# Kernel optimization log

Measured on AMD Instinct MI355X. Metric: run time of the kernel, lower is better.

Reference implementation:

```python
import jax, jax.numpy as jnp
import numpy as np
from jax import lax

B, L, D_MODEL = 4, 1024, 512
D_STATE, D_CONV, D_INNER = 16, 4, 2 * D_MODEL


def setup_inputs() -> dict:
    key = jax.random.key(0)
    ks = jax.random.split(key, 8)
    s = 0.02
    x = jax.random.normal(ks[0], (B, L, D_MODEL), dtype=jnp.float32)
    W_in = jax.random.normal(ks[1], (D_MODEL, 2 * D_INNER), dtype=jnp.float32) * s
    conv_w = jax.random.normal(ks[2], (D_INNER, 1, D_CONV), dtype=jnp.float32) * s  # OIH, depthwise
    conv_b = jnp.zeros((D_INNER,), jnp.float32)
    W_x = jax.random.normal(ks[3], (D_INNER, 2 * D_STATE), dtype=jnp.float32) * s
    W_dt = jax.random.normal(ks[4], (D_INNER, D_INNER), dtype=jnp.float32) * s
    b_dt = jnp.zeros((D_INNER,), jnp.float32)
    # A_log = -logspace(log10(0.001), log10(1.0), d_state); used directly as A in the scan
    A_log = -jnp.logspace(np.log10(1e-3), 0.0, D_STATE, dtype=jnp.float32)
    D_skip = jnp.ones((D_INNER,), jnp.float32) * 0.1
    W_out = jax.random.normal(ks[5], (D_INNER, D_MODEL), dtype=jnp.float32) * s
    gamma = jnp.ones((D_MODEL,), jnp.float32)
    beta = jnp.zeros((D_MODEL,), jnp.float32)
    return dict(x=x, W_in=W_in, conv_w=conv_w, conv_b=conv_b, W_x=W_x, W_dt=W_dt,
                b_dt=b_dt, A_log=A_log, D_skip=D_skip, W_out=W_out, gamma=gamma, beta=beta)


def _mamba_forward(x, W_in, conv_w, conv_b, W_x, W_dt, b_dt, A_log, D_skip, W_out, gamma, beta):
    x = jnp.clip(x, -10.0, 10.0)
    x_and_res = x @ W_in                                  # [B, L, 2*d_inner]
    xp, res = jnp.split(x_and_res, 2, axis=-1)
    # Depthwise causal conv1d: torch pads d_conv-1 both sides then slices [:L] -> left-pad only.
    xt = jnp.transpose(xp, (0, 2, 1))                     # [B, d_inner, L]
    xc = lax.conv_general_dilated(xt, conv_w, window_strides=(1,),
                                  padding=[(D_CONV - 1, 0)],
                                  dimension_numbers=('NCH', 'OIH', 'NCH'),
                                  feature_group_count=D_INNER)
    xc = xc + conv_b[None, :, None]
    xc = jax.nn.silu(jnp.transpose(xc, (0, 2, 1)))        # [B, L, d_inner]
    ssm = xc @ W_x                                        # [B, L, 2*d_state]
    Bm, Cm = jnp.split(ssm, 2, axis=-1)                   # each [B, L, d_state]
    delta = xc @ W_dt + b_dt                              # [B, L, d_inner] (no softplus in source)

    # Selective scan over time (sequential recurrence)
    def step(h, inp):
        u_t, d_t, B_t, C_t = inp                          # [B,I], [B,I], [B,S], [B,S]
        dA = jnp.exp(jnp.clip(d_t[:, :, None] * A_log, -5.0, 5.0))   # [B, I, S]
        h = dA * h + (d_t[:, :, None] * B_t[:, None, :]) * u_t[:, :, None]
        y = jnp.einsum('bis,bs->bi', h, C_t)
        return h, y

    tm = lambda a: jnp.swapaxes(a, 0, 1)                  # time-major
    h0 = jnp.zeros((x.shape[0], D_INNER, D_STATE), xc.dtype)
    _, ys = lax.scan(step, h0, (tm(xc), tm(delta), tm(Bm), tm(Cm)))
    y = jnp.swapaxes(ys, 0, 1) + xc * D_skip              # D skip connection

    y = y * jax.nn.silu(res)                              # gating
    out = y @ W_out
    r = out + x                                           # residual
    mu = jnp.mean(r, axis=-1, keepdims=True)
    var = jnp.var(r, axis=-1, keepdims=True)
    return gamma * (r - mu) / jnp.sqrt(var + 1e-5) + beta


def reference(x, W_in, conv_w, conv_b, W_x, W_dt, b_dt, A_log, D_skip, W_out, gamma, beta):
    return _mamba_forward(x, W_in, conv_w, conv_b, W_x, W_dt, b_dt, A_log, D_skip, W_out, gamma, beta)
```

## Files before the change

### kernel.cpp

```cpp
#include <hip/hip_runtime.h>
#include <hip/hip_bf16.h>

typedef __hip_bfloat16 bf16;
typedef unsigned short ushort_t;
typedef unsigned int uint_t;
typedef __attribute__((ext_vector_type(8))) __bf16 bf16x8;
typedef __attribute__((ext_vector_type(8))) ushort_t u16x8;
typedef __attribute__((ext_vector_type(4))) float f32x4;

#define BB 4
#define LL 1024
#define DM 512
#define DS 16
#define DI 1024
#define ROWS 4096
#define NC 64
#define CT 16
#define NDTX 1152

__device__ __forceinline__ float b2f(bf16 v) { return __bfloat162float(v); }

__device__ __forceinline__ float load_flag(const void* src, int i, int isbf)
{
    return isbf ? b2f(((const bf16*)src)[i]) : ((const float*)src)[i];
}

__device__ __forceinline__ ushort_t f2b_bits(float v)
{
    bf16 t = __float2bfloat16(v);
    return *(ushort_t*)&t;
}

__device__ __forceinline__ float bits2f(ushort_t u)
{
    uint_t w = ((uint_t)u) << 16;
    return __uint_as_float(w);
}

__device__ __forceinline__ int detect_local(const ushort_t* wdt)
{
    __shared__ int bad;
    if (threadIdx.x == 0) bad = 0;
    __syncthreads();
    ushort_t u = wdt[threadIdx.x & 255];
    if (((u >> 7) & 0xFF) >= 127) atomicAdd(&bad, 1);
    __syncthreads();
    return (bad <= 8) ? 1 : 0;
}

__global__ __launch_bounds__(256)
void prep_all(const void* x, const void* Win, const void* Wdt, const void* Wx,
              const void* Wout, const void* cw, const void* cb, const void* Alog,
              const void* Dsk, const void* gam, const void* bet, const void* bdt,
              bf16* __restrict__ xbf, bf16* __restrict__ WtIn,
              bf16* __restrict__ WtDtx, bf16* __restrict__ WtOut,
              float* __restrict__ ccw, float* __restrict__ ccb,
              float* __restrict__ cAlg, float* __restrict__ cDsk,
              float* __restrict__ cgam, float* __restrict__ cbet,
              float* __restrict__ bdtx)
{
    const int isbf = detect_local((const ushort_t*)Wdt);
    int blk = blockIdx.x;

    if (blk < 2048) {
        int idx = blk * 256 + threadIdx.x;
        float v[4];
        if (isbf) {
            uint2 raw = ((const uint2*)x)[idx];
            v[0] = __uint_as_float(raw.x << 16);
            v[1] = __uint_as_float(raw.x & 0xFFFF0000u);
            v[2] = __uint_as_float(raw.y << 16);
            v[3] = __uint_as_float(raw.y & 0xFFFF0000u);
        } else {
            float4 raw = ((const float4*)x)[idx];
            v[0] = raw.x; v[1] = raw.y; v[2] = raw.z; v[3] = raw.w;
        }
        uint_t b0, b1;
        b0 = f2b_bits(fminf(fmaxf(v[0], -10.f), 10.f))
           | ((uint_t)f2b_bits(fminf(fmaxf(v[1], -10.f), 10.f)) << 16);
        b1 = f2b_bits(fminf(fmaxf(v[2], -10.f), 10.f))
           | ((uint_t)f2b_bits(fminf(fmaxf(v[3], -10.f), 10.f)) << 16);
        uint2 ow; ow.x = b0; ow.y = b1;
        ((uint2*)xbf)[idx] = ow;
    } else if (blk < 4640) {
        int tb = blk - 2048;
        const void* src; bf16* dst; int K, Nsrc, tpr;
        if (tb < 1024)      { src = Win;  dst = WtIn;               K = 512;  Nsrc = 2048; tpr = 64; }
        else if (tb < 2048) { tb -= 1024; src = Wdt;  dst = WtDtx;  K = 1024; Nsrc = 1024; tpr = 32; }
        else if (tb < 2080) { tb -= 2048; src = Wx;   dst = WtDtx + 1024 * 1024; K = 1024; Nsrc = 32; tpr = 1; }
        else                { tb -= 2080; src = Wout; dst = WtOut;  K = 1024; Nsrc = 512;  tpr = 16; }
        int k0 = (tb / tpr) * 32, n0 = (tb % tpr) * 32;

        __shared__ float tile[32][33];
        int tx = threadIdx.x & 31, ty = threadIdx.x >> 5;
        #pragma unroll
        for (int j = 0; j < 4; ++j)
            tile[ty + 8 * j][tx] = load_flag(src, (k0 + ty + 8 * j) * Nsrc + n0 + tx, isbf);
        __syncthreads();
        #pragma unroll
        for (int j = 0; j < 4; ++j)
            dst[(size_t)(n0 + ty + 8 * j) * K + k0 + tx] = __float2bfloat16(tile[tx][ty + 8 * j]);
    } else {
        int i = (blk - 4640) * 256 + threadIdx.x;
        if (i < 4096)        ccw[i] = load_flag(cw, i, isbf);
        else if (i < 5120)   ccb[i - 4096] = load_flag(cb, i - 4096, isbf);
        else if (i < 5136)   cAlg[i - 5120] = load_flag(Alog, i - 5120, isbf);
        else if (i < 6160)   cDsk[i - 5136] = load_flag(Dsk, i - 5136, isbf);
        else if (i < 6672)   cgam[i - 6160] = load_flag(gam, i - 6160, isbf);
        else if (i < 7184)   cbet[i - 6672] = load_flag(bet, i - 6672, isbf);
        else if (i < 8336) {
            int j = i - 7184;
            bdtx[j] = (j < DI) ? load_flag(bdt, j, isbf) : 0.f;
        } else if (i < 106640) {
            (WtDtx + 1056 * 1024)[i - 8336] = __float2bfloat16(0.f);
        }
    }
}

__device__ __forceinline__ void gload16(const bf16* g, ushort_t* l)
{
    __builtin_amdgcn_global_load_lds(
        (const __attribute__((address_space(1))) void*)g,
        (__attribute__((address_space(3))) void*)l, 16, 0, 0);
}

template <int TM, int TN, bool OBF>
__global__ __launch_bounds__(256)
void gemm_mfma(const bf16* __restrict__ A, const bf16* __restrict__ Bt,
               const float* __restrict__ bias, void* __restrict__ Cv,
               int M, int N, int K)
{
    constexpr int MI = TM / 32, NJ = TN / 32;
    constexpr int NQA = TM * 8 / 256;
    constexpr int NQB = TN * 8 / 256;
    __shared__ ushort_t As[TM * 64];
    __shared__ ushort_t Bs[TN * 64];

    const int tid = threadIdx.x;
    const int lane = tid & 63;
    const int w = tid >> 6;
    const int wr = w >> 1, wc = w & 1;
    const int m0 = blockIdx.y * TM;
    const int n0 = blockIdx.x * TN;

    const bf16* gA[NQA]; ushort_t* lA[NQA];
    #pragma unroll
    for (int q = 0; q < NQA; ++q) {
        int p = q * 256 + tid;
        int row = p >> 3, kc = ((p & 7) - row) & 7;
        gA[q] = A + (size_t)(m0 + row) * K + kc * 8;
        lA[q] = &As[(q * 256 + w * 64) * 8];
    }
    const bf16* gB[NQB]; ushort_t* lB[NQB];
    #pragma unroll
    for (int q = 0; q < NQB; ++q) {
        int p = q * 256 + tid;
        int row = p >> 3, kc = ((p & 7) - row) & 7;
        gB[q] = Bt + (size_t)(n0 + row) * K + kc * 8;
        lB[q] = &Bs[(q * 256 + w * 64) * 8];
    }

    f32x4 acc[MI][NJ];
    #pragma unroll
    for (int i = 0; i < MI; ++i)
        #pragma unroll
        for (int j = 0; j < NJ; ++j)
            acc[i][j] = (f32x4){0.f, 0.f, 0.f, 0.f};

    const int ko = lane >> 4;
    const int ml = lane & 15;

    for (int k0 = 0; k0 < K; k0 += 64) {
        #pragma unroll
        for (int q = 0; q < NQA; ++q) gload16(gA[q] + k0, lA[q]);
        #pragma unroll
        for (int q = 0; q < NQB; ++q) gload16(gB[q] + k0, lB[q]);
        __syncthreads();

        #pragma unroll
        for (int half = 0; half < 2; ++half) {
            bf16x8 af[MI], bfr[NJ];
            #pragma unroll
            for (int i = 0; i < MI; ++i) {
                int m = wr * (TM / 2) + i * 16 + ml;
                af[i] = *(const bf16x8*)&As[(m * 8 + ((half * 4 + ko + m) & 7)) * 8];
            }
            #pragma unroll
            for (int j = 0; j < NJ; ++j) {
                int n = wc * (TN / 2) + j * 16 + ml;
                bfr[j] = *(const bf16x8*)&Bs[(n * 8 + ((half * 4 + ko + n) & 7)) * 8];
            }
            #pragma unroll
            for (int i = 0; i < MI; ++i)
                #pragma unroll
                for (int j = 0; j < NJ; ++j)
                    acc[i][j] = __builtin_amdgcn_mfma_f32_16x16x32_bf16(
                        af[i], bfr[j], acc[i][j], 0, 0, 0);
        }
        __syncthreads();
    }

    const int rq = lane >> 4;
    #pragma unroll
    for (int j = 0; j < NJ; ++j) {
        int n = n0 + wc * (TN / 2) + j * 16 + ml;
        float bv = bias ? bias[n] : 0.f;
        #pragma unroll
        for (int i = 0; i < MI; ++i) {
            int mb = m0 + wr * (TM / 2) + i * 16 + rq * 4;
            #pragma unroll
            for (int r = 0; r < 4; ++r) {
                float v = acc[i][j][r] + bv;
                if (OBF) ((bf16*)Cv)[(size_t)(mb + r) * N + n] = __float2bfloat16(v);
                else     ((float*)Cv)[(size_t)(mb + r) * N + n] = v;
            }
        }
    }
}

__global__ __launch_bounds__(256)
void conv_silu(const bf16* __restrict__ xrb, const float* __restrict__ cw,
               const float* __restrict__ cb, bf16* __restrict__ xcb)
{
    int idx = blockIdx.x * 256 + threadIdx.x;
    int i = (idx & 127) * 8;
    int row = idx >> 7;
    int t = row & (LL - 1);

    const u16x8 zv = {0, 0, 0, 0, 0, 0, 0, 0};
    const ushort_t* base = (const ushort_t*)(xrb) + (size_t)row * 2048 + i;
    u16x8 r3 = *(const u16x8*)base;
    u16x8 r2 = (t >= 1) ? *(const u16x8*)(base - 2048) : zv;
    u16x8 r1 = (t >= 2) ? *(const u16x8*)(base - 4096) : zv;
    u16x8 r0 = (t >= 3) ? *(const u16x8*)(base - 6144) : zv;

    u16x8 out;
    #pragma unroll
    for (int k = 0; k < 8; ++k) {
        float4 w = ((const float4*)cw)[i + k];
        float acc = cb[i + k];
        acc = fmaf(bits2f(r0[k]), w.x, acc);
        acc = fmaf(bits2f(r1[k]), w.y, acc);
        acc = fmaf(bits2f(r2[k]), w.z, acc);
        acc = fmaf(bits2f(r3[k]), w.w, acc);
        out[k] = f2b_bits(acc / (1.f + __expf(-acc)));
    }
    *(u16x8*)((ushort_t*)xcb + (size_t)row * DI + i) = out;
}

__global__ __launch_bounds__(1024)
void scan_fused(const bf16* __restrict__ xcb, const bf16* __restrict__ dlx,
                const bf16* __restrict__ xrb, const float* __restrict__ A_log,
                const float* __restrict__ Dskip, bf16* __restrict__ ybf)
{
    __shared__ uint_t lsum[DS * NC * 16];

    const int tid = threadIdx.x;
    const int b = blockIdx.x >> 6;
    const int ch0 = (blockIdx.x & 63) << 4;
    const int chl = tid & 15;
    const int c = tid >> 4;
    const int i = ch0 + chl;

    float a[DS];
    #pragma unroll
    for (int s = 0; s < DS; ++s) a[s] = A_log[s];

    const int row0 = b * LL + c * CT;
    float h[DS] = {};
    float p[DS];
    #pragma unroll
    for (int s = 0; s < DS; ++s) p[s] = 1.f;

    for (int t = 0; t < CT; ++t) {
        const size_t row = row0 + t;
        float d = bits2f(((const ushort_t*)dlx)[row * NDTX + i]);
        float u = bits2f(((const ushort_t*)xcb)[row * DI + i]);
        float du = d * u;
        const u16x8* sp = (const u16x8*)(dlx + row * NDTX + 1024);
        u16x8 B0 = sp[0], B1 = sp[1];
        #pragma unroll
        for (int s = 0; s < DS; ++s) {
            float e = fminf(fmaxf(d * a[s], -5.f), 5.f);
            float dA = __expf(e);
            float Bv = bits2f(s < 8 ? B0[s] : B1[s - 8]);
            h[s] = fmaf(dA, h[s], du * Bv);
            p[s] *= dA;
        }
    }
    #pragma unroll
    for (int s = 0; s < DS; ++s)
        lsum[s * 1024 + tid] = (uint_t)f2b_bits(p[s]) | ((uint_t)f2b_bits(h[s]) << 16);
    __syncthreads();

    if (tid < 256) {
        int cl = tid & 15, s = tid >> 4;
        float hh = 0.f;
        for (int cc = 0; cc < NC; ++cc) {
            int off = s * 1024 + cc * 16 + cl;
            uint_t wrd = lsum[off];
            float pp = bits2f((ushort_t)(wrd & 0xFFFF));
            float qq = bits2f((ushort_t)(wrd >> 16));
            lsum[off] = (uint_t)f2b_bits(hh);
            hh = fmaf(pp, hh, qq);
        }
    }
    __syncthreads();

    #pragma unroll
    for (int s = 0; s < DS; ++s) h[s] = bits2f((ushort_t)lsum[s * 1024 + tid]);

    const float dsk = Dskip[i];
    for (int t = 0; t < CT; ++t) {
        const size_t row = row0 + t;
        float d = bits2f(((const ushort_t*)dlx)[row * NDTX + i]);
        float u = bits2f(((const ushort_t*)xcb)[row * DI + i]);
        float du = d * u;
        const u16x8* sp = (const u16x8*)(dlx + row * NDTX + 1024);
        u16x8 B0 = sp[0], B1 = sp[1], C0 = sp[2], C1 = sp[3];
        float y = 0.f;
        #pragma unroll
        for (int s = 0; s < DS; ++s) {
            float e = fminf(fmaxf(d * a[s], -5.f), 5.f);
            float dA = __expf(e);
            float Bv = bits2f(s < 8 ? B0[s] : B1[s - 8]);
            float Cv = bits2f(s < 8 ? C0[s] : C1[s - 8]);
            h[s] = fmaf(dA, h[s], du * Bv);
            y = fmaf(h[s], Cv, y);
        }
        float res = bits2f(((const ushort_t*)xrb)[row * 2048 + DI + i]);
        float g = res / (1.f + __expf(-res));
        ybf[row * DI + i] = __float2bfloat16((y + u * dsk) * g);
    }
}

__global__ __launch_bounds__(256)
void ln_kernel(const float* __restrict__ outp, const void* __restrict__ xsrc,
               const void* __restrict__ wdt_probe,
               const float* __restrict__ gamma, const float* __restrict__ beta,
               void* __restrict__ out)
{
    const int isbf = detect_local((const ushort_t*)wdt_probe);
    const int row = blockIdx.x;
    const int tid = threadIdx.x;

    float r[2];
    float sum = 0.f, ss = 0.f;
    #pragma unroll
    for (int q = 0; q < 2; ++q) {
        int j = tid + q * 256;
        float xv = load_flag(xsrc, row * DM + j, isbf);
        xv = fminf(fmaxf(xv, -10.f), 10.f);
        float v = outp[(size_t)row * DM + j] + xv;
        r[q] = v;
        sum += v;
        ss = fmaf(v, v, ss);
    }
    #pragma unroll
    for (int off = 32; off >= 1; off >>= 1) {
        sum += __shfl_down(sum, off);
        ss  += __shfl_down(ss, off);
    }
    __shared__ float s1[4], s2[4];
    __shared__ float stats[2];
    int wid = tid >> 6, lane = tid & 63;
    if (lane == 0) { s1[wid] = sum; s2[wid] = ss; }
    __syncthreads();
    if (tid == 0) {
        float S = s1[0] + s1[1] + s1[2] + s1[3];
        float Qq = s2[0] + s2[1] + s2[2] + s2[3];
        float mean = S / DM;
        float var = Qq / DM - mean * mean;
        stats[0] = mean;
        stats[1] = rsqrtf(var + 1e-5f);
    }
    __syncthreads();
    float mean = stats[0], rstd = stats[1];
    #pragma unroll
    for (int q = 0; q < 2; ++q) {
        int j = tid + q * 256;
        float v = (r[q] - mean) * rstd * gamma[j] + beta[j];
        size_t o = (size_t)row * DM + j;
        if (isbf) ((bf16*)out)[o] = __float2bfloat16(v);
        else      ((float*)out)[o] = v;
    }
}

extern "C" void kernel_launch(void* const* d_in, const int* in_sizes, int n_in,
                              void* d_out, int out_size, void* d_ws, size_t ws_size,
                              hipStream_t stream)
{
    float* W = (float*)d_ws;
    float* ccw  = W;
    float* ccb  = ccw  + 4096;
    float* cAlg = ccb  + 1024;
    float* cDsk = cAlg + 16;
    float* cgam = cDsk + 1024;
    float* cbet = cgam + 512;
    float* bdtx = cbet + 512;
    float* outp = bdtx + 1152;
    bf16*  xbf  = (bf16*)(outp + 2097152);
    bf16*  xrb  = xbf  + 2097152;
    bf16*  xcb  = xrb  + 8388608;
    bf16*  ybf  = xcb  + 4194304;
    bf16*  dlx  = ybf  + 4194304;
    bf16*  WtIn = dlx  + 4718592;
    bf16*  WtDtx= WtIn + 1048576;
    bf16*  WtOut= WtDtx+ 1179648;

    prep_all<<<5057, 256, 0, stream>>>(
        d_in[0], d_in[1], d_in[5], d_in[4], d_in[9], d_in[2], d_in[3],
        d_in[7], d_in[8], d_in[10], d_in[11], d_in[6],
        xbf, WtIn, WtDtx, WtOut, ccw, ccb, cAlg, cDsk, cgam, cbet, bdtx);

    gemm_mfma<64, 128, true><<<dim3(2048 / 128, ROWS / 64), 256, 0, stream>>>(
        xbf, WtIn, nullptr, xrb, ROWS, 2048, 512);

    conv_silu<<<ROWS * DI / 8 / 256, 256, 0, stream>>>(xrb, ccw, ccb, xcb);

    gemm_mfma<64, 128, true><<<dim3(NDTX / 128, ROWS / 64), 256, 0, stream>>>(
        xcb, WtDtx, bdtx, dlx, ROWS, NDTX, DI);

    scan_fused<<<256, 1024, 0, stream>>>(xcb, dlx, xrb, cAlg, cDsk, ybf);

    gemm_mfma<64, 64, false><<<dim3(DM / 64, ROWS / 64), 256, 0, stream>>>(
        ybf, WtOut, nullptr, outp, ROWS, DM, DI);

    ln_kernel<<<ROWS, 256, 0, stream>>>(outp, d_in[0], d_in[5], cgam, cbet, d_out);
}
```

Measured before the change: 218.0 us.

## Store intermediates channel-major so scan reads contiguous time vectors; split dt/ssm GEMMs

The in-projection and dt GEMMs now write transposed (channel-major) bf16 outputs. The conv kernel reads these along time, and it emits both channel-major and row-major copies through an LDS transpose. The dt projection and the B/C projection become separate GEMMs. The scan loads 16 timesteps of delta, u and the gate as vector loads instead of strided scalar reads. This trades coalesced row stores in the GEMM epilogue for 8-byte strided transposed stores, and adds an extra small GEMM launch and a duplicate xc buffer.

```diff
diff --git a/kernel.cpp b/kernel.cpp
--- a/kernel.cpp
+++ b/kernel.cpp
@@ -6,6 +6,7 @@
 typedef unsigned int uint_t;
 typedef __attribute__((ext_vector_type(8))) __bf16 bf16x8;
 typedef __attribute__((ext_vector_type(8))) ushort_t u16x8;
+typedef __attribute__((ext_vector_type(4))) ushort_t u16x4;
 typedef __attribute__((ext_vector_type(4))) float f32x4;
 
 #define BB 4
@@ -16,7 +17,6 @@
 #define ROWS 4096
 #define NC 64
 #define CT 16
-#define NDTX 1152
 
 __device__ __forceinline__ float b2f(bf16 v) { return __bfloat162float(v); }
 
@@ -51,13 +51,14 @@
 __global__ __launch_bounds__(256)
 void prep_all(const void* x, const void* Win, const void* Wdt, const void* Wx,
               const void* Wout, const void* cw, const void* cb, const void* Alog,
-              const void* Dsk, const void* gam, const void* bet, const void* bdt,
+              const void* Dsk, const void* gam, const void* bet, const void* bdtin,
               bf16* __restrict__ xbf, bf16* __restrict__ WtIn,
-              bf16* __restrict__ WtDtx, bf16* __restrict__ WtOut,
+              bf16* __restrict__ WtDt, bf16* __restrict__ WtSsm,
+              bf16* __restrict__ WtOut,
               float* __restrict__ ccw, float* __restrict__ ccb,
               float* __restrict__ cAlg, float* __restrict__ cDsk,
               float* __restrict__ cgam, float* __restrict__ cbet,
-              float* __restrict__ bdtx)
+              float* __restrict__ bdt)
 {
     const int isbf = detect_local((const ushort_t*)Wdt);
     int blk = blockIdx.x;
@@ -85,10 +86,10 @@
     } else if (blk < 4640) {
         int tb = blk - 2048;
         const void* src; bf16* dst; int K, Nsrc, tpr;
-        if (tb < 1024)      { src = Win;  dst = WtIn;               K = 512;  Nsrc = 2048; tpr = 64; }
-        else if (tb < 2048) { tb -= 1024; src = Wdt;  dst = WtDtx;  K = 1024; Nsrc = 1024; tpr = 32; }
-        else if (tb < 2080) { tb -= 2048; src = Wx;   dst = WtDtx + 1024 * 1024; K = 1024; Nsrc = 32; tpr = 1; }
-        else                { tb -= 2080; src = Wout; dst = WtOut;  K = 1024; Nsrc = 512;  tpr = 16; }
+        if (tb < 1024)      { src = Win;  dst = WtIn;  K = 512;  Nsrc = 2048; tpr = 64; }
+        else if (tb < 2048) { tb -= 1024; src = Wdt;  dst = WtDt;  K = 1024; Nsrc = 1024; tpr = 32; }
+        else if (tb < 2080) { tb -= 2048; src = Wx;   dst = WtSsm; K = 1024; Nsrc = 32;   tpr = 1; }
+        else                { tb -= 2080; src = Wout; dst = WtOut; K = 1024; Nsrc = 512;  tpr = 16; }
         int k0 = (tb / tpr) * 32, n0 = (tb % tpr) * 32;
 
         __shared__ float tile[32][33];
@@ -108,12 +109,8 @@
         else if (i < 6160)   cDsk[i - 5136] = load_flag(Dsk, i - 5136, isbf);
         else if (i < 6672)   cgam[i - 6160] = load_flag(gam, i - 6160, isbf);
         else if (i < 7184)   cbet[i - 6672] = load_flag(bet, i - 6672, isbf);
-        else if (i < 8336) {
-            int j = i - 7184;
-            bdtx[j] = (j < DI) ? load_flag(bdt, j, isbf) : 0.f;
-        } else if (i < 106640) {
-            (WtDtx + 1056 * 1024)[i - 8336] = __float2bfloat16(0.f);
-        }
+        else if (i < 8208)   bdt[i - 7184] = load_flag(bdtin, i - 7184, isbf);
+        else if (i < 40976)  (WtSsm + 32 * 1024)[i - 8208] = __float2bfloat16(0.f);
     }
 }
 
@@ -124,7 +121,7 @@
         (__attribute__((address_space(3))) void*)l, 16, 0, 0);
 }
 
-template <int TM, int TN, bool OBF>
+template <int TM, int TN, bool OBF, bool OT>
 __global__ __launch_bounds__(256)
 void gemm_mfma(const bf16* __restrict__ A, const bf16* __restrict__ Bt,
                const float* __restrict__ bias, void* __restrict__ Cv,
@@ -208,50 +205,81 @@
         #pragma unroll
         for (int i = 0; i < MI; ++i) {
             int mb = m0 + wr * (TM / 2) + i * 16 + rq * 4;
-            #pragma unroll
-            for (int r = 0; r < 4; ++r) {
-                float v = acc[i][j][r] + bv;
-                if (OBF) ((bf16*)Cv)[(size_t)(mb + r) * N + n] = __float2bfloat16(v);
-                else     ((float*)Cv)[(size_t)(mb + r) * N + n] = v;
+            if (OT) {
+                u16x4 pk;
+                #pragma unroll
+                for (int r = 0; r < 4; ++r)
+                    pk[r] = f2b_bits(acc[i][j][r] + bv);
+                *(u16x4*)((ushort_t*)Cv + (size_t)n * M + mb) = pk;
+            } else {
+                #pragma unroll
+                for (int r = 0; r < 4; ++r) {
+                    float v = acc[i][j][r] + bv;
+                    if (OBF) ((bf16*)Cv)[(size_t)(mb + r) * N + n] = __float2bfloat16(v);
+                    else     ((float*)Cv)[(size_t)(mb + r) * N + n] = v;
+                }
             }
         }
     }
 }
 
 __global__ __launch_bounds__(256)
-void conv_silu(const bf16* __restrict__ xrb, const float* __restrict__ cw,
-               const float* __restrict__ cb, bf16* __restrict__ xcb)
-{
-    int idx = blockIdx.x * 256 + threadIdx.x;
-    int i = (idx & 127) * 8;
-    int row = idx >> 7;
-    int t = row & (LL - 1);
-
-    const u16x8 zv = {0, 0, 0, 0, 0, 0, 0, 0};
-    const ushort_t* base = (const ushort_t*)(xrb) + (size_t)row * 2048 + i;
-    u16x8 r3 = *(const u16x8*)base;
-    u16x8 r2 = (t >= 1) ? *(const u16x8*)(base - 2048) : zv;
-    u16x8 r1 = (t >= 2) ? *(const u16x8*)(base - 4096) : zv;
-    u16x8 r0 = (t >= 3) ? *(const u16x8*)(base - 6144) : zv;
-
-    u16x8 out;
-    #pragma unroll
-    for (int k = 0; k < 8; ++k) {
-        float4 w = ((const float4*)cw)[i + k];
-        float acc = cb[i + k];
-        acc = fmaf(bits2f(r0[k]), w.x, acc);
-        acc = fmaf(bits2f(r1[k]), w.y, acc);
-        acc = fmaf(bits2f(r2[k]), w.z, acc);
-        acc = fmaf(bits2f(r3[k]), w.w, acc);
-        out[k] = f2b_bits(acc / (1.f + __expf(-acc)));
-    }
-    *(u16x8*)((ushort_t*)xcb + (size_t)row * DI + i) = out;
+void conv_silu(const bf16* __restrict__ xrbT, const float* __restrict__ cw,
+               const float* __restrict__ cb, bf16* __restrict__ xcT,
+               bf16* __restrict__ xc)
+{
+    __shared__ ushort_t tile[64 * 72];
+    const int blk = blockIdx.x;
+    const int ch0 = (blk & 15) * 64;
+    const int T0b = (blk >> 4) * 64;
+    const int lc = threadIdx.x >> 2, tg = threadIdx.x & 3;
+    const int i = ch0 + lc;
+    const int T0 = T0b + tg * 16;
+
+    const ushort_t* base = (const ushort_t*)xrbT + (size_t)i * ROWS + T0;
+    u16x8 m0 = *(const u16x8*)base;
+    u16x8 m1 = *(const u16x8*)(base + 8);
+    u16x8 pv = {0, 0, 0, 0, 0, 0, 0, 0};
+    if ((T0 & (LL - 1)) != 0) pv = *(const u16x8*)(base - 8);
+
+    float4 w = ((const float4*)cw)[i];
+    float bs = cb[i];
+    float xm3 = bits2f(pv[5]), xm2 = bits2f(pv[6]), xm1 = bits2f(pv[7]);
+    u16x8 o0, o1;
+    #pragma unroll
+    for (int tt = 0; tt < 16; ++tt) {
+        float x0 = bits2f(tt < 8 ? m0[tt] : m1[tt - 8]);
+        float acc = bs;
+        acc = fmaf(xm3, w.x, acc);
+        acc = fmaf(xm2, w.y, acc);
+        acc = fmaf(xm1, w.z, acc);
+        acc = fmaf(x0,  w.w, acc);
+        ushort_t ob = f2b_bits(acc / (1.f + __expf(-acc)));
+        if (tt < 8) o0[tt] = ob; else o1[tt - 8] = ob;
+        xm3 = xm2; xm2 = xm1; xm1 = x0;
+    }
+    ushort_t* dt = (ushort_t*)xcT + (size_t)i * ROWS + T0;
+    *(u16x8*)dt = o0;
+    *(u16x8*)(dt + 8) = o1;
+    *(u16x8*)&tile[lc * 72 + tg * 16] = o0;
+    *(u16x8*)&tile[lc * 72 + tg * 16 + 8] = o1;
+    __syncthreads();
+    const int lt = threadIdx.x >> 2, cg = threadIdx.x & 3;
+    u16x8 q0, q1;
+    #pragma unroll
+    for (int j = 0; j < 8; ++j) q0[j] = tile[(cg * 16 + j) * 72 + lt];
+    #pragma unroll
+    for (int j = 8; j < 16; ++j) q1[j - 8] = tile[(cg * 16 + j) * 72 + lt];
+    ushort_t* wp = (ushort_t*)xc + (size_t)(T0b + lt) * DI + ch0 + cg * 16;
+    *(u16x8*)wp = q0;
+    *(u16x8*)(wp + 8) = q1;
 }
 
 __global__ __launch_bounds__(1024)
-void scan_fused(const bf16* __restrict__ xcb, const bf16* __restrict__ dlx,
-                const bf16* __restrict__ xrb, const float* __restrict__ A_log,
-                const float* __restrict__ Dskip, bf16* __restrict__ ybf)
+void scan_fused(const bf16* __restrict__ xcT, const bf16* __restrict__ dT,
+                const bf16* __restrict__ ssm, const bf16* __restrict__ xrbT,
+                const float* __restrict__ A_log, const float* __restrict__ Dskip,
+                bf16* __restrict__ ybf)
 {
     __shared__ uint_t lsum[DS * NC * 16];
 
@@ -261,27 +289,35 @@
     const int chl = tid & 15;
     const int c = tid >> 4;
     const int i = ch0 + chl;
+    const size_t tb = (size_t)b * LL + c * CT;
 
     float a[DS];
     #pragma unroll
     for (int s = 0; s < DS; ++s) a[s] = A_log[s];
 
-    const int row0 = b * LL + c * CT;
+    u16x8 d0, d1, u0, u1;
+    {
+        const u16x8* dp = (const u16x8*)((const ushort_t*)dT + (size_t)i * ROWS + tb);
+        d0 = dp[0]; d1 = dp[1];
+        const u16x8* up = (const u16x8*)((const ushort_t*)xcT + (size_t)i * ROWS + tb);
+        u0 = up[0]; u1 = up[1];
+    }
+
     float h[DS] = {};
     float p[DS];
     #pragma unroll
     for (int s = 0; s < DS; ++s) p[s] = 1.f;
 
+    #pragma unroll
     for (int t = 0; t < CT; ++t) {
-        const size_t row = row0 + t;
-        float d = bits2f(((const ushort_t*)dlx)[row * NDTX + i]);
-        float u = bits2f(((const ushort_t*)xcb)[row * DI + i]);
-        float du = d * u;
-        const u16x8* sp = (const u16x8*)(dlx + row * NDTX + 1024);
+        float dv = bits2f(t < 8 ? d0[t] : d1[t - 8]);
+        float uv = bits2f(t < 8 ? u0[t] : u1[t - 8]);
+        float du = dv * uv;
+        const u16x8* sp = (const u16x8*)((const ushort_t*)ssm + (tb + t) * 64);
         u16x8 B0 = sp[0], B1 = sp[1];
         #pragma unroll
         for (int s = 0; s < DS; ++s) {
-            float e = fminf(fmaxf(d * a[s], -5.f), 5.f);
+            float e = fminf(fmaxf(dv * a[s], -5.f), 5.f);
             float dA = __expf(e);
             float Bv = bits2f(s < 8 ? B0[s] : B1[s - 8]);
             h[s] = fmaf(dA, h[s], du * Bv);
@@ -310,27 +346,33 @@
     #pragma unroll
     for (int s = 0; s < DS; ++s) h[s] = bits2f((ushort_t)lsum[s * 1024 + tid]);
 
+    u16x8 r0, r1;
+    {
+        const u16x8* rp = (const u16x8*)((const ushort_t*)xrbT + (size_t)(1024 + i) * ROWS + tb);
+        r0 = rp[0]; r1 = rp[1];
+    }
     const float dsk = Dskip[i];
+
+    #pragma unroll
     for (int t = 0; t < CT; ++t) {
-        const size_t row = row0 + t;
-        float d = bits2f(((const ushort_t*)dlx)[row * NDTX + i]);
-        float u = bits2f(((const ushort_t*)xcb)[row * DI + i]);
-        float du = d * u;
-        const u16x8* sp = (const u16x8*)(dlx + row * NDTX + 1024);
+        float dv = bits2f(t < 8 ? d0[t] : d1[t - 8]);
+        float uv = bits2f(t < 8 ? u0[t] : u1[t - 8]);
+        float du = dv * uv;
+        const u16x8* sp = (const u16x8*)((const ushort_t*)ssm + (tb + t) * 64);
         u16x8 B0 = sp[0], B1 = sp[1], C0 = sp[2], C1 = sp[3];
         float y = 0.f;
         #pragma unroll
         for (int s = 0; s < DS; ++s) {
-            float e = fminf(fmaxf(d * a[s], -5.f), 5.f);
+            float e = fminf(fmaxf(dv * a[s], -5.f), 5.f);
             float dA = __expf(e);
             float Bv = bits2f(s < 8 ? B0[s] : B1[s - 8]);
-            float Cv = bits2f(s < 8 ? C0[s] : C1[s - 8]);
+            float Cc = bits2f(s < 8 ? C0[s] : C1[s - 8]);
             h[s] = fmaf(dA, h[s], du * Bv);
-            y = fmaf(h[s], Cv, y);
-        }
-        float res = bits2f(((const ushort_t*)xrb)[row * 2048 + DI + i]);
+            y = fmaf(h[s], Cc, y);
+        }
+        float res = bits2f(t < 8 ? r0[t] : r1[t - 8]);
         float g = res / (1.f + __expf(-res));
-        ybf[row * DI + i] = __float2bfloat16((y + u * dsk) * g);
+        ybf[(tb + t) * DI + i] = __float2bfloat16((y + uv * dsk) * g);
     }
 }
 
@@ -397,33 +439,39 @@
     float* cDsk = cAlg + 16;
     float* cgam = cDsk + 1024;
     float* cbet = cgam + 512;
-    float* bdtx = cbet + 512;
-    float* outp = bdtx + 1152;
+    float* bdt  = cbet + 512;
+    float* outp = bdt  + 1024;
     bf16*  xbf  = (bf16*)(outp + 2097152);
-    bf16*  xrb  = xbf  + 2097152;
-    bf16*  xcb  = xrb  + 8388608;
-    bf16*  ybf  = xcb  + 4194304;
-    bf16*  dlx  = ybf  + 4194304;
-    bf16*  WtIn = dlx  + 4718592;
-    bf16*  WtDtx= WtIn + 1048576;
-    bf16*  WtOut= WtDtx+ 1179648;
-
-    prep_all<<<5057, 256, 0, stream>>>(
+    bf16*  xrbT = xbf  + 2097152;
+    bf16*  xcT  = xrbT + 8388608;
+    bf16*  xc   = xcT  + 4194304;
+    bf16*  ybf  = xc   + 4194304;
+    bf16*  dT   = ybf  + 4194304;
+    bf16*  ssm  = dT   + 4194304;
+    bf16*  WtIn = ssm  + 262144;
+    bf16*  WtDt = WtIn + 1048576;
+    bf16*  WtSsm= WtDt + 1048576;
+    bf16*  WtOut= WtSsm+ 65536;
+
+    prep_all<<<4801, 256, 0, stream>>>(
         d_in[0], d_in[1], d_in[5], d_in[4], d_in[9], d_in[2], d_in[3],
         d_in[7], d_in[8], d_in[10], d_in[11], d_in[6],
-        xbf, WtIn, WtDtx, WtOut, ccw, ccb, cAlg, cDsk, cgam, cbet, bdtx);
-
-    gemm_mfma<64, 128, true><<<dim3(2048 / 128, ROWS / 64), 256, 0, stream>>>(
-        xbf, WtIn, nullptr, xrb, ROWS, 2048, 512);
-
-    conv_silu<<<ROWS * DI / 8 / 256, 256, 0, stream>>>(xrb, ccw, ccb, xcb);
-
-    gemm_mfma<64, 128, true><<<dim3(NDTX / 128, ROWS / 64), 256, 0, stream>>>(
-        xcb, WtDtx, bdtx, dlx, ROWS, NDTX, DI);
-
-    scan_fused<<<256, 1024, 0, stream>>>(xcb, dlx, xrb, cAlg, cDsk, ybf);
-
-    gemm_mfma<64, 64, false><<<dim3(DM / 64, ROWS / 64), 256, 0, stream>>>(
+        xbf, WtIn, WtDt, WtSsm, WtOut, ccw, ccb, cAlg, cDsk, cgam, cbet, bdt);
+
+    gemm_mfma<64, 128, true, true><<<dim3(2048 / 128, ROWS / 64), 256, 0, stream>>>(
+        xbf, WtIn, nullptr, xrbT, ROWS, 2048, 512);
+
+    conv_silu<<<1024, 256, 0, stream>>>(xrbT, ccw, ccb, xcT, xc);
+
+    gemm_mfma<64, 128, true, true><<<dim3(DI / 128, ROWS / 64), 256, 0, stream>>>(
+        xc, WtDt, bdt, dT, ROWS, DI, DI);
+
+    gemm_mfma<32, 64, true, false><<<dim3(1, ROWS / 32), 256, 0, stream>>>(
+        xc, WtSsm, nullptr, ssm, ROWS, 64, DI);
+
+    scan_fused<<<256, 1024, 0, stream>>>(xcT, dT, ssm, xrbT, cAlg, cDsk, ybf);
+
+    gemm_mfma<64, 64, false, false><<<dim3(DM / 64, ROWS / 64), 256, 0, stream>>>(
         ybf, WtOut, nullptr, outp, ROWS, DM, DI);
 
     ln_kernel<<<ROWS, 256, 0, stream>>>(outp, d_in[0], d_in[5], cgam, cbet, d_out);
```

Result: slower. 463.0 us (+112.4%).
